# Kernel optimization log

Measured on AMD Instinct MI355X. Metric: run time of the kernel, lower is better.

The kernel has to match this reference:

```python
import jax, jax.numpy as jnp
import numpy as np

B, H, S, D = 2, 16, 2048, 64
NUM_BUCKETS = 32
MAX_DISTANCE = 256


def setup_inputs() -> dict:
    key = jax.random.key(0)
    kq, kk, kv, kb, kl = jax.random.split(key, 5)
    q = jax.random.normal(kq, (B, H, S, D), dtype=jnp.float32)
    k = jax.random.normal(kk, (B, H, S, D), dtype=jnp.float32)
    v = jax.random.normal(kv, (B, H, S, D), dtype=jnp.float32)
    bias_table = jax.random.normal(kb, (NUM_BUCKETS, H), dtype=jnp.float32)
    event_length = jax.random.randint(kl, (B,), 1, S + 1, dtype=jnp.int64)
    return {"q": q, "k": k, "v": v, "bias_table": bias_table, "event_length": event_length}


def _relative_position_bucket(relative_position):
    # T5-style bucketing exactly as the torch module: n = -rel_pos
    half = NUM_BUCKETS // 2  # 16
    n = -relative_position
    is_small = n < half
    # guard log for the branch not taken (n<=0); where() masks it out
    nf = jnp.maximum(n, 1).astype(jnp.float32)
    val_if_large = half + jnp.minimum(
        jnp.log(nf / half) / np.log(MAX_DISTANCE / half) * (NUM_BUCKETS - half),
        NUM_BUCKETS - 1 - half,
    ).astype(jnp.int32)
    ret = jnp.where(is_small, n, val_if_large)
    return jnp.clip(ret, 0, NUM_BUCKETS - 1)


def _compute_bias(bias_table, seq_len):
    ctx = jnp.arange(seq_len)[:, None]
    mem = jnp.arange(seq_len)[None, :]
    rp_bucket = _relative_position_bucket(mem - ctx)  # (S,S)
    values = bias_table[rp_bucket]                    # (S,S,H)
    return jnp.transpose(values, (2, 0, 1))[None]     # (1,H,S,S)


def reference(q, k, v, bias_table, event_length):
    seq_len = q.shape[2]
    head_dim = q.shape[3]
    # scaled QK^T: (B,H,S,S)
    logits = jnp.einsum("bhsd,bhtd->bhst", q, k) / np.sqrt(head_dim).astype(np.float32)
    logits = logits + _compute_bias(bias_table, seq_len)
    # key-side padding mask from per-event lengths
    mask = jnp.arange(seq_len)[None, None, None, :] < event_length[:, None, None, None]
    logits = jnp.where(mask, logits, jnp.float32(-1e9))
    attn = jax.nn.softmax(logits, axis=-1)
    # dropout p=0.01 omitted (eval-mode deterministic reference)
    return jnp.einsum("bhst,bhtd->bhsd", attn, v)
```

## Files before the change

### kernel.cpp

```cpp
#include <hip/hip_runtime.h>
#include <hip/hip_bf16.h>

#define B_ 2
#define H_ 16
#define S_ 2048
#define D_ 64
#define BQ 128
#define BK 64
#define LDSTR 72
#define LOG2E 1.4426950408889634f
#define FIXM 10.0f

#if __has_builtin(__builtin_amdgcn_exp2f)
#define EXP2F(x) __builtin_amdgcn_exp2f(x)
#else
#define EXP2F(x) __expf((x) * 0.6931471805599453f)
#endif

typedef _Float16 half8 __attribute__((ext_vector_type(8)));
typedef _Float16 half4 __attribute__((ext_vector_type(4)));
typedef __fp16   fp16x2 __attribute__((ext_vector_type(2)));
typedef float floatx4 __attribute__((ext_vector_type(4)));

__global__ __launch_bounds__(256, 2)
void t5_attn_kernel(const float* __restrict__ qg_, const float* __restrict__ kg_,
                    const float* __restrict__ vg_, const float* __restrict__ bt,
                    const int* __restrict__ elen, float* __restrict__ outg_)
{
    __shared__ __align__(16) _Float16 Kl[2][BK][LDSTR];
    __shared__ __align__(16) _Float16 Vt[2][D_][LDSTR];
    __shared__ __align__(16) _Float16 Pl[4][32][LDSTR];
    __shared__ float lut[256];

    const int qblk = blockIdx.x;
    const int h    = blockIdx.y;
    const int b    = blockIdx.z;
    const int tid  = threadIdx.x;
    const int wave = tid >> 6;
    const int lane = tid & 63;
    const int quad = lane >> 4;
    const int t16  = lane & 15;

    {
        int n = tid;
        int bucket;
        if (n < 16) {
            bucket = n;
        } else {
            int vl = (int)(__log2f((float)n * 0.0625f) * 4.0f);
            bucket = 16 + (vl < 15 ? vl : 15);
        }
        lut[n] = bt[bucket * H_ + h] * LOG2E - FIXM;
    }
    const float sh_next = FIXM - bt[h] * LOG2E;
    const float sh_far  = FIXM - bt[31 * H_ + h] * LOG2E;

    const int len = (elen[1] == 0) ? elen[2 * b] : elen[b];
    const int ntiles = (len + BK - 1) >> 6;

    const size_t bh = ((size_t)b * H_ + h) * (size_t)(S_ * D_);
    const float* qg = qg_ + bh;
    const float* kg = kg_ + bh;
    const float* vg = vg_ + bh;
    float*       og = outg_ + bh;

    half8 qf[2][2];
    #pragma unroll
    for (int rg = 0; rg < 2; ++rg) {
        const float qscale = 0.125f * LOG2E;
        const int row = qblk * BQ + wave * 32 + rg * 16 + t16;
        const float* qp = qg + (size_t)row * D_ + quad * 8;
        #pragma unroll
        for (int c = 0; c < 2; ++c) {
            const float4* p = reinterpret_cast<const float4*>(qp + c * 32);
            float4 x0 = p[0], x1 = p[1];
            half8 hv;
            hv[0] = (_Float16)(x0.x * qscale); hv[1] = (_Float16)(x0.y * qscale);
            hv[2] = (_Float16)(x0.z * qscale); hv[3] = (_Float16)(x0.w * qscale);
            hv[4] = (_Float16)(x1.x * qscale); hv[5] = (_Float16)(x1.y * qscale);
            hv[6] = (_Float16)(x1.z * qscale); hv[7] = (_Float16)(x1.w * qscale);
            qf[rg][c] = hv;
        }
    }

    floatx4 zero4 = {0.f, 0.f, 0.f, 0.f};
    floatx4 acc[2][4];
    float l_[2];
    #pragma unroll
    for (int rg = 0; rg < 2; ++rg) {
        #pragma unroll
        for (int nb = 0; nb < 4; ++nb) acc[rg][nb] = zero4;
        l_[rg] = 0.f;
    }

    const int i_lo = qblk * BQ + wave * 32;

    float4 kx[2][2];
    float  vx[16];
    auto prefetch = [&](int kt) {
        #pragma unroll
        for (int it = 0; it < 2; ++it) {
            int idx = tid + it * 256;
            int row = idx >> 3;
            int c8  = (idx & 7) << 3;
            const float4* p = reinterpret_cast<const float4*>(
                kg + ((size_t)(kt * BK + row) * D_ + c8));
            kx[it][0] = p[0];
            kx[it][1] = p[1];
        }
        #pragma unroll
        for (int it = 0; it < 2; ++it) {
            int key8 = kt * BK + wave * 8 + it * 32;
            #pragma unroll
            for (int jj = 0; jj < 8; ++jj)
                vx[it * 8 + jj] = vg[(size_t)(key8 + jj) * D_ + lane];
        }
    };
    auto stage = [&](int buf) {
        #pragma unroll
        for (int it = 0; it < 2; ++it) {
            int idx = tid + it * 256;
            int row = idx >> 3;
            int c8  = (idx & 7) << 3;
            float4 x0 = kx[it][0], x1 = kx[it][1];
            half8 hv;
            hv[0]=(_Float16)x0.x; hv[1]=(_Float16)x0.y; hv[2]=(_Float16)x0.z; hv[3]=(_Float16)x0.w;
            hv[4]=(_Float16)x1.x; hv[5]=(_Float16)x1.y; hv[6]=(_Float16)x1.z; hv[7]=(_Float16)x1.w;
            *reinterpret_cast<half8*>(&Kl[buf][row][c8]) = hv;
        }
        #pragma unroll
        for (int it = 0; it < 2; ++it) {
            int key8 = wave * 8 + it * 32;
            half8 hv;
            #pragma unroll
            for (int jj = 0; jj < 8; ++jj) hv[jj] = (_Float16)vx[it * 8 + jj];
            *reinterpret_cast<half8*>(&Vt[buf][lane][key8]) = hv;
        }
    };

    prefetch(0);
    stage(0);
    __syncthreads();

    for (int kt = 0; kt < ntiles; ++kt) {
        const int cur = kt & 1;
        const bool more = (kt + 1) < ntiles;
        if (more) prefetch(kt + 1);

        floatx4 sa[2][4];
        #pragma unroll
        for (int rg = 0; rg < 2; ++rg)
            #pragma unroll
            for (int nb = 0; nb < 4; ++nb) sa[rg][nb] = zero4;
        #pragma unroll
        for (int kc = 0; kc < 2; ++kc) {
            #pragma unroll
            for (int nb = 0; nb < 4; ++nb) {
                half8 af = *reinterpret_cast<const half8*>(
                    &Kl[cur][nb * 16 + t16][kc * 32 + quad * 8]);
                sa[0][nb] = __builtin_amdgcn_mfma_f32_16x16x32_f16(af, qf[0][kc], sa[0][nb], 0, 0, 0);
                sa[1][nb] = __builtin_amdgcn_mfma_f32_16x16x32_f16(af, qf[1][kc], sa[1][nb], 0, 0, 0);
            }
        }

        const int base = kt * BK;
        if (i_lo + 31 <= base) {
            #pragma unroll
            for (int rg = 0; rg < 2; ++rg)
                #pragma unroll
                for (int nb = 0; nb < 4; ++nb)
                    #pragma unroll
                    for (int r = 0; r < 4; ++r) sa[rg][nb][r] -= sh_next;
        } else if (i_lo >= base + 279) {
            #pragma unroll
            for (int rg = 0; rg < 2; ++rg)
                #pragma unroll
                for (int nb = 0; nb < 4; ++nb)
                    #pragma unroll
                    for (int r = 0; r < 4; ++r) sa[rg][nb][r] -= sh_far;
        } else {
            #pragma unroll
            for (int rg = 0; rg < 2; ++rg) {
                const int d0 = i_lo + rg * 16 + t16 - base - quad * 4;
                #pragma unroll
                for (int nb = 0; nb < 4; ++nb) {
                    #pragma unroll
                    for (int r = 0; r < 4; ++r) {
                        int d = d0 - nb * 16 - r;
                        d = d < 0 ? 0 : (d > 255 ? 255 : d);
                        sa[rg][nb][r] += lut[d];
                    }
                }
            }
        }
        if ((kt == ntiles - 1) && (len & 63)) {
            #pragma unroll
            for (int nb = 0; nb < 4; ++nb) {
                #pragma unroll
                for (int r = 0; r < 4; ++r) {
                    bool valid = (base + nb * 16 + quad * 4 + r) < len;
                    #pragma unroll
                    for (int rg = 0; rg < 2; ++rg)
                        sa[rg][nb][r] = valid ? sa[rg][nb][r] : -1e30f;
                }
            }
        }

        #pragma unroll
        for (int rg = 0; rg < 2; ++rg) {
            float s = 0.f;
            #pragma unroll
            for (int nb = 0; nb < 4; ++nb)
                #pragma unroll
                for (int r = 0; r < 4; ++r) {
                    sa[rg][nb][r] = EXP2F(sa[rg][nb][r]);
                    s += sa[rg][nb][r];
                }
            l_[rg] += s;
        }

        #pragma unroll
        for (int rg = 0; rg < 2; ++rg) {
            #pragma unroll
            for (int nb = 0; nb < 4; ++nb) {
                fp16x2 lo = __builtin_amdgcn_cvt_pkrtz(sa[rg][nb][0], sa[rg][nb][1]);
                fp16x2 hi = __builtin_amdgcn_cvt_pkrtz(sa[rg][nb][2], sa[rg][nb][3]);
                half4 w;
                w[0] = (_Float16)lo[0]; w[1] = (_Float16)lo[1];
                w[2] = (_Float16)hi[0]; w[3] = (_Float16)hi[1];
                *reinterpret_cast<half4*>(
                    &Pl[wave][rg * 16 + t16][nb * 16 + quad * 4]) = w;
            }
        }
        asm volatile("s_waitcnt lgkmcnt(0)" ::: "memory");

        #pragma unroll
        for (int kc = 0; kc < 2; ++kc) {
            half8 a0 = *reinterpret_cast<const half8*>(
                &Pl[wave][t16][kc * 32 + quad * 8]);
            half8 a1 = *reinterpret_cast<const half8*>(
                &Pl[wave][16 + t16][kc * 32 + quad * 8]);
            #pragma unroll
            for (int nb = 0; nb < 4; ++nb) {
                half8 bv = *reinterpret_cast<const half8*>(
                    &Vt[cur][nb * 16 + t16][kc * 32 + quad * 8]);
                acc[0][nb] = __builtin_amdgcn_mfma_f32_16x16x32_f16(a0, bv, acc[0][nb], 0, 0, 0);
                acc[1][nb] = __builtin_amdgcn_mfma_f32_16x16x32_f16(a1, bv, acc[1][nb], 0, 0, 0);
            }
        }

        if (more) stage(cur ^ 1);
        __syncthreads();
    }

    #pragma unroll
    for (int rg = 0; rg < 2; ++rg) {
        float lv = l_[rg];
        lv += __shfl_xor(lv, 16, 64);
        lv += __shfl_xor(lv, 32, 64);
        float inv = 1.f / lv;
        #pragma unroll
        for (int r = 0; r < 4; ++r) {
            int rowloc = quad * 4 + r;
            float invr = __shfl(inv, (lane & 48) | rowloc, 64);
            const int row = qblk * BQ + wave * 32 + rg * 16 + rowloc;
            #pragma unroll
            for (int nb = 0; nb < 4; ++nb)
                og[(size_t)row * D_ + nb * 16 + t16] = acc[rg][nb][r] * invr;
        }
    }
}

extern "C" void kernel_launch(void* const* d_in, const int* in_sizes, int n_in,
                              void* d_out, int out_size, void* d_ws, size_t ws_size,
                              hipStream_t stream) {
    const float* q  = (const float*)d_in[0];
    const float* k  = (const float*)d_in[1];
    const float* v  = (const float*)d_in[2];
    const float* bt = (const float*)d_in[3];
    const int*   el = (const int*)d_in[4];
    float* out = (float*)d_out;
    dim3 grid(S_ / BQ, H_, B_);
    t5_attn_kernel<<<grid, 256, 0, stream>>>(q, k, v, bt, el, out);
}
```

Measured before the change: 130.9 us.

## Split key tiles across wave pairs and remap blocks for L2 locality

```diff
diff --git a/kernel.cpp b/kernel.cpp
--- a/kernel.cpp
+++ b/kernel.cpp
@@ -1,5 +1,4 @@
 #include <hip/hip_runtime.h>
-#include <hip/hip_bf16.h>
 
 #define B_ 2
 #define H_ 16
@@ -7,6 +6,7 @@
 #define D_ 64
 #define BQ 128
 #define BK 64
+#define NQB (S_ / BQ)
 #define LDSTR 72
 #define LOG2E 1.4426950408889634f
 #define FIXM 10.0f
@@ -22,26 +22,42 @@
 typedef __fp16   fp16x2 __attribute__((ext_vector_type(2)));
 typedef float floatx4 __attribute__((ext_vector_type(4)));
 
-__global__ __launch_bounds__(256, 2)
+typedef _Float16 KlArr[BK][LDSTR];
+typedef _Float16 VtArr[D_][LDSTR];
+typedef _Float16 PlArr[32][LDSTR];
+
+#define VT_OFF  18432
+#define PL_OFF  36864
+#define LUT_OFF 55296
+#define OX_STR  66
+#define LX_OFF  33792
+
+__global__ __launch_bounds__(512, 4)
 void t5_attn_kernel(const float* __restrict__ qg_, const float* __restrict__ kg_,
                     const float* __restrict__ vg_, const float* __restrict__ bt,
                     const int* __restrict__ elen, float* __restrict__ outg_)
 {
-    __shared__ __align__(16) _Float16 Kl[2][BK][LDSTR];
-    __shared__ __align__(16) _Float16 Vt[2][D_][LDSTR];
-    __shared__ __align__(16) _Float16 Pl[4][32][LDSTR];
-    __shared__ float lut[256];
-
-    const int qblk = blockIdx.x;
-    const int h    = blockIdx.y;
-    const int b    = blockIdx.z;
+    __shared__ __align__(16) unsigned char smem[56320];
+    KlArr* Kl  = reinterpret_cast<KlArr*>(smem);
+    VtArr* Vt  = reinterpret_cast<VtArr*>(smem + VT_OFF);
+    PlArr* Pl  = reinterpret_cast<PlArr*>(smem + PL_OFF);
+    float* lut = reinterpret_cast<float*>(smem + LUT_OFF);
+
     const int tid  = threadIdx.x;
     const int wave = tid >> 6;
     const int lane = tid & 63;
     const int quad = lane >> 4;
     const int t16  = lane & 15;
-
-    {
+    const int wq   = wave >> 1;
+    const int kh   = wave & 1;
+
+    const int f    = blockIdx.x + NQB * (blockIdx.y + H_ * blockIdx.z);
+    const int qblk = (f >> 3) & 15;
+    const int bh   = (f & 7) | ((f >> 7) << 3);
+    const int h    = bh & 15;
+    const int b    = bh >> 4;
+
+    if (tid < 256) {
         int n = tid;
         int bucket;
         if (n < 16) {
@@ -58,28 +74,30 @@
     const int len = (elen[1] == 0) ? elen[2 * b] : elen[b];
     const int ntiles = (len + BK - 1) >> 6;
 
-    const size_t bh = ((size_t)b * H_ + h) * (size_t)(S_ * D_);
-    const float* qg = qg_ + bh;
-    const float* kg = kg_ + bh;
-    const float* vg = vg_ + bh;
-    float*       og = outg_ + bh;
+    const size_t bhoff = ((size_t)b * H_ + h) * (size_t)(S_ * D_);
+    const float* qptr = qg_ + bhoff;
+    const float* kptr = kg_ + bhoff;
+    const float* vptr = vg_ + bhoff;
+    float*       optr = outg_ + bhoff;
 
     half8 qf[2][2];
-    #pragma unroll
-    for (int rg = 0; rg < 2; ++rg) {
+    {
         const float qscale = 0.125f * LOG2E;
-        const int row = qblk * BQ + wave * 32 + rg * 16 + t16;
-        const float* qp = qg + (size_t)row * D_ + quad * 8;
-        #pragma unroll
-        for (int c = 0; c < 2; ++c) {
-            const float4* p = reinterpret_cast<const float4*>(qp + c * 32);
-            float4 x0 = p[0], x1 = p[1];
-            half8 hv;
-            hv[0] = (_Float16)(x0.x * qscale); hv[1] = (_Float16)(x0.y * qscale);
-            hv[2] = (_Float16)(x0.z * qscale); hv[3] = (_Float16)(x0.w * qscale);
-            hv[4] = (_Float16)(x1.x * qscale); hv[5] = (_Float16)(x1.y * qscale);
-            hv[6] = (_Float16)(x1.z * qscale); hv[7] = (_Float16)(x1.w * qscale);
-            qf[rg][c] = hv;
+        #pragma unroll
+        for (int rg = 0; rg < 2; ++rg) {
+            const int row = qblk * BQ + wq * 32 + rg * 16 + t16;
+            const float* qp = qptr + (size_t)row * D_ + quad * 8;
+            #pragma unroll
+            for (int c = 0; c < 2; ++c) {
+                const float4* p = reinterpret_cast<const float4*>(qp + c * 32);
+                float4 x0 = p[0], x1 = p[1];
+                half8 hv;
+                hv[0] = (_Float16)(x0.x * qscale); hv[1] = (_Float16)(x0.y * qscale);
+                hv[2] = (_Float16)(x0.z * qscale); hv[3] = (_Float16)(x0.w * qscale);
+                hv[4] = (_Float16)(x1.x * qscale); hv[5] = (_Float16)(x1.y * qscale);
+                hv[6] = (_Float16)(x1.z * qscale); hv[7] = (_Float16)(x1.w * qscale);
+                qf[rg][c] = hv;
+            }
         }
     }
 
@@ -93,49 +111,33 @@
         l_[rg] = 0.f;
     }
 
-    const int i_lo = qblk * BQ + wave * 32;
-
-    float4 kx[2][2];
-    float  vx[16];
+    const int i_lo = qblk * BQ + wq * 32;
+
+    float4 kx[2];
+    float  vx[8];
     auto prefetch = [&](int kt) {
-        #pragma unroll
-        for (int it = 0; it < 2; ++it) {
-            int idx = tid + it * 256;
-            int row = idx >> 3;
-            int c8  = (idx & 7) << 3;
-            const float4* p = reinterpret_cast<const float4*>(
-                kg + ((size_t)(kt * BK + row) * D_ + c8));
-            kx[it][0] = p[0];
-            kx[it][1] = p[1];
-        }
-        #pragma unroll
-        for (int it = 0; it < 2; ++it) {
-            int key8 = kt * BK + wave * 8 + it * 32;
-            #pragma unroll
-            for (int jj = 0; jj < 8; ++jj)
-                vx[it * 8 + jj] = vg[(size_t)(key8 + jj) * D_ + lane];
-        }
+        const int row = tid >> 3;
+        const int c8  = (tid & 7) << 3;
+        const float4* p = reinterpret_cast<const float4*>(
+            kptr + ((size_t)(kt * BK + row) * D_ + c8));
+        kx[0] = p[0];
+        kx[1] = p[1];
+        const int key8 = kt * BK + wave * 8;
+        #pragma unroll
+        for (int jj = 0; jj < 8; ++jj)
+            vx[jj] = vptr[(size_t)(key8 + jj) * D_ + lane];
     };
     auto stage = [&](int buf) {
-        #pragma unroll
-        for (int it = 0; it < 2; ++it) {
-            int idx = tid + it * 256;
-            int row = idx >> 3;
-            int c8  = (idx & 7) << 3;
-            float4 x0 = kx[it][0], x1 = kx[it][1];
-            half8 hv;
-            hv[0]=(_Float16)x0.x; hv[1]=(_Float16)x0.y; hv[2]=(_Float16)x0.z; hv[3]=(_Float16)x0.w;
-            hv[4]=(_Float16)x1.x; hv[5]=(_Float16)x1.y; hv[6]=(_Float16)x1.z; hv[7]=(_Float16)x1.w;
-            *reinterpret_cast<half8*>(&Kl[buf][row][c8]) = hv;
-        }
-        #pragma unroll
-        for (int it = 0; it < 2; ++it) {
-            int key8 = wave * 8 + it * 32;
-            half8 hv;
-            #pragma unroll
-            for (int jj = 0; jj < 8; ++jj) hv[jj] = (_Float16)vx[it * 8 + jj];
-            *reinterpret_cast<half8*>(&Vt[buf][lane][key8]) = hv;
-        }
+        const int row = tid >> 3;
+        const int c8  = (tid & 7) << 3;
+        half8 hv;
+        hv[0]=(_Float16)kx[0].x; hv[1]=(_Float16)kx[0].y; hv[2]=(_Float16)kx[0].z; hv[3]=(_Float16)kx[0].w;
+        hv[4]=(_Float16)kx[1].x; hv[5]=(_Float16)kx[1].y; hv[6]=(_Float16)kx[1].z; hv[7]=(_Float16)kx[1].w;
+        *reinterpret_cast<half8*>(&Kl[buf][row][c8]) = hv;
+        half8 vv;
+        #pragma unroll
+        for (int jj = 0; jj < 8; ++jj) vv[jj] = (_Float16)vx[jj];
+        *reinterpret_cast<half8*>(&Vt[buf][lane][wave * 8]) = vv;
     };
 
     prefetch(0);
@@ -147,43 +149,44 @@
         const bool more = (kt + 1) < ntiles;
         if (more) prefetch(kt + 1);
 
-        floatx4 sa[2][4];
+        const int keybase = kt * BK + kh * 32;
+
+        floatx4 sa[2][2];
         #pragma unroll
         for (int rg = 0; rg < 2; ++rg)
             #pragma unroll
-            for (int nb = 0; nb < 4; ++nb) sa[rg][nb] = zero4;
+            for (int nb = 0; nb < 2; ++nb) sa[rg][nb] = zero4;
         #pragma unroll
         for (int kc = 0; kc < 2; ++kc) {
             #pragma unroll
-            for (int nb = 0; nb < 4; ++nb) {
+            for (int nb = 0; nb < 2; ++nb) {
                 half8 af = *reinterpret_cast<const half8*>(
-                    &Kl[cur][nb * 16 + t16][kc * 32 + quad * 8]);
+                    &Kl[cur][kh * 32 + nb * 16 + t16][kc * 32 + quad * 8]);
                 sa[0][nb] = __builtin_amdgcn_mfma_f32_16x16x32_f16(af, qf[0][kc], sa[0][nb], 0, 0, 0);
                 sa[1][nb] = __builtin_amdgcn_mfma_f32_16x16x32_f16(af, qf[1][kc], sa[1][nb], 0, 0, 0);
             }
         }
 
-        const int base = kt * BK;
-        if (i_lo + 31 <= base) {
+        if (i_lo + 31 <= keybase) {
             #pragma unroll
             for (int rg = 0; rg < 2; ++rg)
                 #pragma unroll
-                for (int nb = 0; nb < 4; ++nb)
+                for (int nb = 0; nb < 2; ++nb)
                     #pragma unroll
                     for (int r = 0; r < 4; ++r) sa[rg][nb][r] -= sh_next;
-        } else if (i_lo >= base + 279) {
+        } else if (i_lo >= keybase + 247) {
             #pragma unroll
             for (int rg = 0; rg < 2; ++rg)
                 #pragma unroll
-                for (int nb = 0; nb < 4; ++nb)
+                for (int nb = 0; nb < 2; ++nb)
                     #pragma unroll
                     for (int r = 0; r < 4; ++r) sa[rg][nb][r] -= sh_far;
         } else {
             #pragma unroll
             for (int rg = 0; rg < 2; ++rg) {
-                const int d0 = i_lo + rg * 16 + t16 - base - quad * 4;
-                #pragma unroll
-                for (int nb = 0; nb < 4; ++nb) {
+                const int d0 = i_lo + rg * 16 + t16 - keybase - quad * 4;
+                #pragma unroll
+                for (int nb = 0; nb < 2; ++nb) {
                     #pragma unroll
                     for (int r = 0; r < 4; ++r) {
                         int d = d0 - nb * 16 - r;
@@ -195,10 +198,10 @@
         }
         if ((kt == ntiles - 1) && (len & 63)) {
             #pragma unroll
-            for (int nb = 0; nb < 4; ++nb) {
+            for (int nb = 0; nb < 2; ++nb) {
                 #pragma unroll
                 for (int r = 0; r < 4; ++r) {
-                    bool valid = (base + nb * 16 + quad * 4 + r) < len;
+                    bool valid = (keybase + nb * 16 + quad * 4 + r) < len;
                     #pragma unroll
                     for (int rg = 0; rg < 2; ++rg)
                         sa[rg][nb][r] = valid ? sa[rg][nb][r] : -1e30f;
@@ -210,7 +213,7 @@
         for (int rg = 0; rg < 2; ++rg) {
             float s = 0.f;
             #pragma unroll
-            for (int nb = 0; nb < 4; ++nb)
+            for (int nb = 0; nb < 2; ++nb)
                 #pragma unroll
                 for (int r = 0; r < 4; ++r) {
                     sa[rg][nb][r] = EXP2F(sa[rg][nb][r]);
@@ -222,28 +225,27 @@
         #pragma unroll
         for (int rg = 0; rg < 2; ++rg) {
             #pragma unroll
-            for (int nb = 0; nb < 4; ++nb) {
+            for (int nb = 0; nb < 2; ++nb) {
                 fp16x2 lo = __builtin_amdgcn_cvt_pkrtz(sa[rg][nb][0], sa[rg][nb][1]);
                 fp16x2 hi = __builtin_amdgcn_cvt_pkrtz(sa[rg][nb][2], sa[rg][nb][3]);
                 half4 w;
                 w[0] = (_Float16)lo[0]; w[1] = (_Float16)lo[1];
                 w[2] = (_Float16)hi[0]; w[3] = (_Float16)hi[1];
                 *reinterpret_cast<half4*>(
-                    &Pl[wave][rg * 16 + t16][nb * 16 + quad * 4]) = w;
+                    &Pl[wq][rg * 16 + t16][kh * 32 + nb * 16 + quad * 4]) = w;
             }
         }
         asm volatile("s_waitcnt lgkmcnt(0)" ::: "memory");
 
-        #pragma unroll
-        for (int kc = 0; kc < 2; ++kc) {
+        {
             half8 a0 = *reinterpret_cast<const half8*>(
-                &Pl[wave][t16][kc * 32 + quad * 8]);
+                &Pl[wq][t16][kh * 32 + quad * 8]);
             half8 a1 = *reinterpret_cast<const half8*>(
-                &Pl[wave][16 + t16][kc * 32 + quad * 8]);
+                &Pl[wq][16 + t16][kh * 32 + quad * 8]);
             #pragma unroll
             for (int nb = 0; nb < 4; ++nb) {
                 half8 bv = *reinterpret_cast<const half8*>(
-                    &Vt[cur][nb * 16 + t16][kc * 32 + quad * 8]);
+                    &Vt[cur][nb * 16 + t16][kh * 32 + quad * 8]);
                 acc[0][nb] = __builtin_amdgcn_mfma_f32_16x16x32_f16(a0, bv, acc[0][nb], 0, 0, 0);
                 acc[1][nb] = __builtin_amdgcn_mfma_f32_16x16x32_f16(a1, bv, acc[1][nb], 0, 0, 0);
             }
@@ -253,20 +255,44 @@
         __syncthreads();
     }
 
+    float lh[2];
     #pragma unroll
     for (int rg = 0; rg < 2; ++rg) {
         float lv = l_[rg];
         lv += __shfl_xor(lv, 16, 64);
         lv += __shfl_xor(lv, 32, 64);
-        float inv = 1.f / lv;
-        #pragma unroll
-        for (int r = 0; r < 4; ++r) {
-            int rowloc = quad * 4 + r;
-            float invr = __shfl(inv, (lane & 48) | rowloc, 64);
-            const int row = qblk * BQ + wave * 32 + rg * 16 + rowloc;
+        lh[rg] = lv;
+    }
+    float* Ox = reinterpret_cast<float*>(smem);
+    float* Lx = reinterpret_cast<float*>(smem + LX_OFF);
+    if (kh == 1) {
+        #pragma unroll
+        for (int rg = 0; rg < 2; ++rg) {
             #pragma unroll
             for (int nb = 0; nb < 4; ++nb)
-                og[(size_t)row * D_ + nb * 16 + t16] = acc[rg][nb][r] * invr;
+                #pragma unroll
+                for (int r = 0; r < 4; ++r)
+                    Ox[(wq * 32 + rg * 16 + quad * 4 + r) * OX_STR + nb * 16 + t16] =
+                        acc[rg][nb][r];
+            if (quad == 0) Lx[wq * 32 + rg * 16 + t16] = lh[rg];
+        }
+    }
+    __syncthreads();
+    if (kh == 0) {
+        #pragma unroll
+        for (int rg = 0; rg < 2; ++rg) {
+            const float inv = 1.f / (lh[rg] + Lx[wq * 32 + rg * 16 + t16]);
+            #pragma unroll
+            for (int r = 0; r < 4; ++r) {
+                const int rowloc = quad * 4 + r;
+                const float invr = __shfl(inv, (lane & 48) | rowloc, 64);
+                const int row = qblk * BQ + wq * 32 + rg * 16 + rowloc;
+                #pragma unroll
+                for (int nb = 0; nb < 4; ++nb)
+                    optr[(size_t)row * D_ + nb * 16 + t16] =
+                        (acc[rg][nb][r] +
+                         Ox[(wq * 32 + rg * 16 + rowloc) * OX_STR + nb * 16 + t16]) * invr;
+            }
         }
     }
 }
@@ -280,6 +306,6 @@
     const float* bt = (const float*)d_in[3];
     const int*   el = (const int*)d_in[4];
     float* out = (float*)d_out;
-    dim3 grid(S_ / BQ, H_, B_);
-    t5_attn_kernel<<<grid, 256, 0, stream>>>(q, k, v, bt, el, out);
+    dim3 grid(NQB, H_, B_);
+    t5_attn_kernel<<<grid, 512, 0, stream>>>(q, k, v, bt, el, out);
 }
```

After: 121.9 us. -6.9%, faster.
